# Kernel optimization log

Measured on AMD Instinct MI355X. Metric: run time of the kernel, lower is better.

Reference implementation:

```python
import jax, jax.numpy as jnp
import numpy as np

B, S, H, V, NH, FF, M, NL = 16, 512, 256, 8000, 4, 512, 64, 2
BETA, THR, ALPHA = 0.9, 1.0, 2.0  # snn.Leaky defaults: beta=0.9, threshold=1.0, ATan surrogate alpha=2


@jax.custom_vjp
def spike(u):
    return (u > 0).astype(u.dtype)

def _spike_fwd(u):
    return (u > 0).astype(u.dtype), u

def _spike_bwd(u, g):
    # snntorch ATan surrogate gradient
    return (g * (ALPHA / 2.0) / (1.0 + (jnp.pi * u * ALPHA / 2.0) ** 2),)

spike.defvjp(_spike_fwd, _spike_bwd)


def layer_norm(x, g, b):
    m = x.mean(-1, keepdims=True)
    v = ((x - m) ** 2).mean(-1, keepdims=True)
    return (x - m) / jnp.sqrt(v + 1e-5) * g + b


def mha(x, wqkv, bqkv, wo, bo):
    Bx, Sx, Hx = x.shape
    hd = Hx // NH
    qkv = x @ wqkv.T + bqkv
    q, k, v = jnp.split(qkv, 3, axis=-1)
    sp = lambda t: t.reshape(Bx, Sx, NH, hd).transpose(0, 2, 1, 3)
    q, k, v = sp(q), sp(k), sp(v)
    att = jax.nn.softmax(jnp.einsum('bhqd,bhkd->bhqk', q, k) / (float(hd) ** 0.5), axis=-1)
    o = jnp.einsum('bhqk,bhkd->bhqd', att, v).transpose(0, 2, 1, 3).reshape(Bx, Sx, Hx)
    return o @ wo.T + bo


def spiking_worker(x, w, b):
    # batched projection for all timesteps, then a single-pass LIF scan
    proj = x @ w.T + b  # [B,S,H]

    def step(mem, xt):
        reset = spike(mem - THR)              # spike detected from previous membrane
        mem = BETA * mem + xt - reset * THR   # subtract-reset mechanism
        return mem, spike(mem - THR)

    mem0 = jnp.zeros((x.shape[0], x.shape[2]), x.dtype)
    _, spks = jax.lax.scan(step, mem0, jnp.swapaxes(proj, 0, 1))
    return jnp.swapaxes(spks, 0, 1)  # [B,S,H]


def _forward(input_ids, embed, pos, qkv_w, qkv_b, out_w, out_b, ln1_g, ln1_b,
             ff1_w, ff1_b, ff2_w, ff2_b, ln2_g, ln2_b,
             log_w, log_b, mat_w, mat_b, conv_w, conv_b,
             read_w, read_b, memory, head_w, head_b):
    x = embed[input_ids] + pos[:, :input_ids.shape[1], :]
    for i in range(NL):  # post-norm TransformerEncoderLayer x2, gelu, eval mode
        x = layer_norm(x + mha(x, qkv_w[i], qkv_b[i], out_w[i], out_b[i]), ln1_g[i], ln1_b[i])
        h = jax.nn.gelu(x @ ff1_w[i].T + ff1_b[i], approximate=False) @ ff2_w[i].T + ff2_b[i]
        x = layer_norm(x + h, ln2_g[i], ln2_b[i])
    plan = x
    logico = spiking_worker(plan, log_w, log_b)
    matem = spiking_worker(plan, mat_w, mat_b)
    ling = jax.lax.conv_general_dilated(
        jnp.swapaxes(plan, 1, 2), conv_w, (1,), [(1, 1)],
        dimension_numbers=('NCH', 'OIH', 'NCH')) + conv_b[None, :, None]
    ling = jnp.swapaxes(ling, 1, 2)
    combined = jnp.concatenate([logico, matem, ling, plan], axis=-1)  # [B,S,4H]
    plan_mean = plan.mean(axis=1)                                      # [B,H]
    read_weights = jax.nn.softmax(plan_mean @ read_w.T + read_b, axis=-1)
    memory_read = read_weights @ memory                                # [B,H]
    logits = combined @ head_w.T + head_b                              # [B,S,V]
    return logits, memory_read


def setup_inputs() -> dict:
    key = jax.random.key(0)
    ks = iter(jax.random.split(key, 32))
    sc = 0.02
    rn = lambda shape, s=sc: jax.random.normal(next(ks), shape, jnp.float32) * s
    inp = {
        'input_ids': jax.random.randint(next(ks), (B, S), 0, V),
        'embed': rn((V, H), 1.0),
        'pos': rn((1, 512, H), 1.0),
        'qkv_w': rn((NL, 3 * H, H)), 'qkv_b': rn((NL, 3 * H)),
        'out_w': rn((NL, H, H)), 'out_b': rn((NL, H)),
        'ln1_g': jnp.ones((NL, H), jnp.float32), 'ln1_b': jnp.zeros((NL, H), jnp.float32),
        'ff1_w': rn((NL, FF, H)), 'ff1_b': rn((NL, FF)),
        'ff2_w': rn((NL, H, FF)), 'ff2_b': rn((NL, H)),
        'ln2_g': jnp.ones((NL, H), jnp.float32), 'ln2_b': jnp.zeros((NL, H), jnp.float32),
        'log_w': rn((H, H)), 'log_b': rn((H,)),
        'mat_w': rn((H, H)), 'mat_b': rn((H,)),
        'conv_w': rn((H, H, 3)), 'conv_b': rn((H,)),
        'read_w': rn((M, H)), 'read_b': rn((M,)),
        'memory': rn((M, H), 1.0),
        'head_w': rn((V, 4 * H)), 'head_b': rn((V,)),
    }
    return inp


def reference(input_ids, embed, pos, qkv_w, qkv_b, out_w, out_b, ln1_g, ln1_b,
              ff1_w, ff1_b, ff2_w, ff2_b, ln2_g, ln2_b,
              log_w, log_b, mat_w, mat_b, conv_w, conv_b,
              read_w, read_b, memory, head_w, head_b):
    return _forward(input_ids, embed, pos, qkv_w, qkv_b, out_w, out_b, ln1_g, ln1_b,
                    ff1_w, ff1_b, ff2_w, ff2_b, ln2_g, ln2_b,
                    log_w, log_b, mat_w, mat_b, conv_w, conv_b,
                    read_w, read_b, memory, head_w, head_b)
```

## Files before the change

### kernel.cpp

```cpp
#include <hip/hip_runtime.h>
#include <hip/hip_bf16.h>

constexpr int Bc = 16, Sc = 512, Hc = 256, Vc = 8000, NHc = 4, HDc = 64;
constexpr int FFc = 512, Mc = 64;
constexpr int ROWS = Bc * Sc;
constexpr int CH = 4 * Hc;
constexpr int NT2 = CH / 32;

typedef __attribute__((ext_vector_type(4))) float f32x4v;
typedef __attribute__((ext_vector_type(8))) short short8v;
typedef __hip_bfloat16 bf16;

__device__ inline void split3(float x, bf16& h, bf16& m, bf16& l) {
    h = __float2bfloat16(x);
    const float r = x - __bfloat162float(h);
    m = __float2bfloat16(r);
    const float r2 = r - __bfloat162float(m);
    l = __float2bfloat16(r2);
}

__device__ __forceinline__ void split_range(const float* __restrict__ in,
                                            bf16* __restrict__ h, bf16* __restrict__ m,
                                            bf16* __restrict__ l, int blk, int t) {
    const size_t i = ((size_t)blk * 256 + t) * 4;
    const float4 v = *(const float4*)&in[i];
    split3(v.x, h[i + 0], m[i + 0], l[i + 0]);
    split3(v.y, h[i + 1], m[i + 1], l[i + 1]);
    split3(v.z, h[i + 2], m[i + 2], l[i + 2]);
    split3(v.w, h[i + 3], m[i + 3], l[i + 3]);
}

__global__ __launch_bounds__(256) void k_prep(
    const float* __restrict__ qkv_w, const float* __restrict__ out_w,
    const float* __restrict__ ff1_w, const float* __restrict__ ff2_w,
    const float* __restrict__ log_w, const float* __restrict__ mat_w,
    const float* __restrict__ conv_w, const float* __restrict__ head_w,
    const float* __restrict__ log_b, const float* __restrict__ mat_b,
    bf16* qkvwh, bf16* qkvwm, bf16* qkvwl,
    bf16* outwh, bf16* outwm, bf16* outwl,
    bf16* ff1wh, bf16* ff1wm, bf16* ff1wl,
    bf16* ff2wh, bf16* ff2wm, bf16* ff2wl,
    bf16* lmwh, bf16* lmwm, bf16* lmwl,
    bf16* w2h, bf16* w2m, bf16* w2l,
    bf16* hwb, float* lmb) {
    const int blk = blockIdx.x;
    const int t = threadIdx.x;
    if (blk < 384) {
        split_range(qkv_w, qkvwh, qkvwm, qkvwl, blk, t);
    } else if (blk < 512) {
        split_range(out_w, outwh, outwm, outwl, blk - 384, t);
    } else if (blk < 768) {
        split_range(ff1_w, ff1wh, ff1wm, ff1wl, blk - 512, t);
    } else if (blk < 1024) {
        split_range(ff2_w, ff2wh, ff2wm, ff2wl, blk - 768, t);
    } else if (blk < 1088) {
        split_range(log_w, lmwh, lmwm, lmwl, blk - 1024, t);
    } else if (blk < 1152) {
        split_range(mat_w, lmwh + 65536, lmwm + 65536, lmwl + 65536, blk - 1088, t);
    } else if (blk < 1920) {
        const int idx = (blk - 1152) * 256 + t;
        const int o = idx / 768, rem = idx % 768;
        const int k = rem >> 8, i = rem & 255;
        split3(conv_w[(size_t)o * 768 + i * 3 + k], w2h[idx], w2m[idx], w2l[idx]);
    } else if (blk < 9920) {
        const size_t i = ((size_t)(blk - 1920) * 256 + t) * 4;
        const float4 v = *(const float4*)&head_w[i];
        hwb[i + 0] = __float2bfloat16(v.x);
        hwb[i + 1] = __float2bfloat16(v.y);
        hwb[i + 2] = __float2bfloat16(v.z);
        hwb[i + 3] = __float2bfloat16(v.w);
    } else {
        lmb[t] = log_b[t];
        lmb[256 + t] = mat_b[t];
    }
}

__global__ __launch_bounds__(256) void k_embed(const int* __restrict__ ids,
                                               const float* __restrict__ emb,
                                               const float* __restrict__ pos,
                                               float* __restrict__ x,
                                               bf16* __restrict__ xh, bf16* __restrict__ xm,
                                               bf16* __restrict__ xl) {
    const int r = blockIdx.x;
    const int h = threadIdx.x;
    const int s = r & (Sc - 1);
    const int id = ids[r];
    const float v = emb[(size_t)id * Hc + h] + pos[(size_t)s * Hc + h];
    const size_t o = (size_t)r * Hc + h;
    x[o] = v;
    split3(v, xh[o], xm[o], xl[o]);
}

template <int EPI, int OUTS, int BN>
__global__ __launch_bounds__(256) void k_bg3(
    const bf16* __restrict__ Ah, const bf16* __restrict__ Am, const bf16* __restrict__ Al,
    const bf16* __restrict__ Bh, const bf16* __restrict__ Bm, const bf16* __restrict__ Bl,
    const float* __restrict__ bias, float* __restrict__ C,
    bf16* __restrict__ Oh, bf16* __restrict__ Om, bf16* __restrict__ Ol,
    int K, int lda, int ldb, int ldc,
    long zA2, long zA1, long zB2, long zB1, long zC2, long zC1) {
    constexpr int NF = BN / 32;
    __shared__ bf16 As[3][128 * 32];
    __shared__ bf16 Bs[3][BN * 32];
    const int z = blockIdx.z, z2 = z >> 2, z1 = z & 3;
    const size_t aoff = (size_t)z2 * zA2 + (size_t)z1 * zA1;
    const size_t boff = (size_t)z2 * zB2 + (size_t)z1 * zB1;
    const size_t coff = (size_t)z2 * zC2 + (size_t)z1 * zC1;
    const int t = threadIdx.x;
    const int tm = blockIdx.x * 128, tn = blockIdx.y * BN;
    const int w = t >> 6, l = t & 63;
    const int wr = w >> 1, wc = w & 1;
    const bf16* Ap[3] = {Ah, Am, Al};
    const bf16* Bp[3] = {Bh, Bm, Bl};
    f32x4v acc[4][NF];
    const f32x4v zero = {0.f, 0.f, 0.f, 0.f};
#pragma unroll
    for (int i = 0; i < 4; ++i)
#pragma unroll
        for (int j = 0; j < NF; ++j) acc[i][j] = zero;

    for (int kt = 0; kt < K; kt += 32) {
#pragma unroll
        for (int p = 0; p < 3; ++p) {
#pragma unroll
            for (int j = 0; j < 2; ++j) {
                const int c = j * 256 + t;
                const int row = c >> 2, kc = c & 3;
                const int skc = kc ^ ((row >> 1) & 3);
                const bf16* ga = Ap[p] + aoff + (size_t)(tm + row) * lda + kt + skc * 8;
                __builtin_amdgcn_global_load_lds((const __attribute__((address_space(1))) void*)ga,
                                                 (__attribute__((address_space(3))) void*)(&As[p][0] + c * 8),
                                                 16, 0, 0);
            }
            if (BN == 128) {
#pragma unroll
                for (int j = 0; j < 2; ++j) {
                    const int c = j * 256 + t;
                    const int row = c >> 2, kc = c & 3;
                    const int skc = kc ^ ((row >> 1) & 3);
                    const bf16* gb = Bp[p] + boff + (size_t)(tn + row) * ldb + kt + skc * 8;
                    __builtin_amdgcn_global_load_lds((const __attribute__((address_space(1))) void*)gb,
                                                     (__attribute__((address_space(3))) void*)(&Bs[p][0] + c * 8),
                                                     16, 0, 0);
                }
            } else {
                const int c = t;
                const int row = c >> 2, kc = c & 3;
                const int skc = kc ^ ((row >> 1) & 3);
                const bf16* gb = Bp[p] + boff + (size_t)(tn + row) * ldb + kt + skc * 8;
                __builtin_amdgcn_global_load_lds((const __attribute__((address_space(1))) void*)gb,
                                                 (__attribute__((address_space(3))) void*)(&Bs[p][0] + c * 8),
                                                 16, 0, 0);
            }
        }
        __syncthreads();
        const int lr = l & 15, lkc = l >> 4;
        short8v af[3][4], bfr[3][NF];
#pragma unroll
        for (int p = 0; p < 3; ++p)
#pragma unroll
            for (int m = 0; m < 4; ++m) {
                const int row = wr * 64 + m * 16 + lr;
                const int sc = lkc ^ ((row >> 1) & 3);
                af[p][m] = *(const short8v*)(&As[p][0] + row * 32 + sc * 8);
            }
#pragma unroll
        for (int p = 0; p < 3; ++p)
#pragma unroll
            for (int n = 0; n < NF; ++n) {
                const int row = wc * (BN / 2) + n * 16 + lr;
                const int sc = lkc ^ ((row >> 1) & 3);
                bfr[p][n] = *(const short8v*)(&Bs[p][0] + row * 32 + sc * 8);
            }
#pragma unroll
        for (int m = 0; m < 4; ++m)
#pragma unroll
            for (int n = 0; n < NF; ++n)
                acc[m][n] = __builtin_amdgcn_mfma_f32_16x16x32_bf16(af[0][m], bfr[0][n], acc[m][n], 0, 0, 0);
#pragma unroll
        for (int m = 0; m < 4; ++m)
#pragma unroll
            for (int n = 0; n < NF; ++n)
                acc[m][n] = __builtin_amdgcn_mfma_f32_16x16x32_bf16(af[0][m], bfr[1][n], acc[m][n], 0, 0, 0);
#pragma unroll
        for (int m = 0; m < 4; ++m)
#pragma unroll
            for (int n = 0; n < NF; ++n)
                acc[m][n] = __builtin_amdgcn_mfma_f32_16x16x32_bf16(af[1][m], bfr[0][n], acc[m][n], 0, 0, 0);
#pragma unroll
        for (int m = 0; m < 4; ++m)
#pragma unroll
            for (int n = 0; n < NF; ++n)
                acc[m][n] = __builtin_amdgcn_mfma_f32_16x16x32_bf16(af[0][m], bfr[2][n], acc[m][n], 0, 0, 0);
#pragma unroll
        for (int m = 0; m < 4; ++m)
#pragma unroll
            for (int n = 0; n < NF; ++n)
                acc[m][n] = __builtin_amdgcn_mfma_f32_16x16x32_bf16(af[2][m], bfr[0][n], acc[m][n], 0, 0, 0);
#pragma unroll
        for (int m = 0; m < 4; ++m)
#pragma unroll
            for (int n = 0; n < NF; ++n)
                acc[m][n] = __builtin_amdgcn_mfma_f32_16x16x32_bf16(af[1][m], bfr[1][n], acc[m][n], 0, 0, 0);
        __syncthreads();
    }
    const int lr = l & 15, lq = (l >> 4) * 4;
#pragma unroll
    for (int n = 0; n < NF; ++n) {
        const int col = tn + wc * (BN / 2) + n * 16 + lr;
        const float bv = (EPI == 0 || EPI == 1) ? bias[col] : 0.0f;
#pragma unroll
        for (int m = 0; m < 4; ++m) {
            const int rbase = tm + wr * 64 + m * 16 + lq;
#pragma unroll
            for (int j = 0; j < 4; ++j) {
                float v = acc[m][n][j];
                if (EPI == 0) v += bv;
                if (EPI == 1) { v += bv; v = 0.5f * v * (1.0f + erff(v / 1.41421356237309515f)); }
                const size_t o = coff + (size_t)(rbase + j) * ldc + col;
                if (OUTS == 0) C[o] = v;
                else if (OUTS == 3) ((bf16*)C)[o] = __float2bfloat16(v);
                else split3(v, Oh[o], Om[o], Ol[o]);
            }
        }
    }
}

__global__ __launch_bounds__(256) void k_vt(const bf16* __restrict__ qh,
                                            const bf16* __restrict__ qm,
                                            const bf16* __restrict__ ql,
                                            bf16* __restrict__ vh, bf16* __restrict__ vm,
                                            bf16* __restrict__ vl) {
    __shared__ bf16 tile[64][72];
    const int sblk = blockIdx.x;
    const int z = blockIdx.y;
    const int b = z >> 2, h = z & 3;
    const int t = threadIdx.x;
    const int sr = t >> 2, c16 = (t & 3) * 16;
    const bf16* qp[3] = {qh, qm, ql};
    bf16* vp[3] = {vh, vm, vl};
    for (int p = 0; p < 3; ++p) {
        const bf16* src = qp[p] + (size_t)(b * Sc + sblk * 64 + sr) * 768 + 512 + h * 64 + c16;
        *(short8v*)&tile[sr][c16] = *(const short8v*)src;
        *(short8v*)&tile[sr][c16 + 8] = *(const short8v*)(src + 8);
        __syncthreads();
        bf16 out[16];
#pragma unroll
        for (int i = 0; i < 16; ++i) out[i] = tile[c16 + i][sr];
        bf16* dst = vp[p] + (size_t)(z * 64 + sr) * Sc + sblk * 64 + c16;
        *(short8v*)dst = *(short8v*)&out[0];
        *(short8v*)(dst + 8) = *(short8v*)&out[8];
        __syncthreads();
    }
}

#define S_PASS(QA, KB)                                                                     \
    _Pragma("unroll") for (int m = 0; m < 2; ++m) _Pragma("unroll") for (int ks = 0; ks < 2; ++ks) \
        sa[m] = __builtin_amdgcn_mfma_f32_16x16x32_bf16(QA[m][ks], KB[ks], sa[m], 0, 0, 0);
#define PV_PASS(PA, VB)                                                                    \
    _Pragma("unroll") for (int m = 0; m < 2; ++m) _Pragma("unroll") for (int ks = 0; ks < 2; ++ks) \
        oa[m] = __builtin_amdgcn_mfma_f32_16x16x32_bf16(PA[m][ks], VB[ks], oa[m], 0, 0, 0);

__global__ __launch_bounds__(512) void k_attn(
    const bf16* __restrict__ qph, const bf16* __restrict__ qpm, const bf16* __restrict__ qpl,
    const bf16* __restrict__ vth, const bf16* __restrict__ vtm, const bf16* __restrict__ vtl,
    bf16* __restrict__ oh, bf16* __restrict__ om, bf16* __restrict__ ol) {
    extern __shared__ char smem[];
    float* S = (float*)smem;
    bf16* KV0 = (bf16*)(smem + 131072);
    bf16* KV1 = KV0 + 4096;
    bf16* KV2 = KV1 + 4096;
    const int qc = blockIdx.x, z = blockIdx.y;
    const int b = z >> 2, hh = z & 3;
    const int t = threadIdx.x;
    const int w = t >> 6, lane = t & 63;
    const int lr = lane & 15, lkc = lane >> 4;
    const int qg = w >> 2, kg = w & 3;
    const int r8 = t >> 3, c8 = t & 7;
    const f32x4v zero = {0.f, 0.f, 0.f, 0.f};

    short8v qf0[2][2], qf1[2][2], qf2[2][2];
#pragma unroll
    for (int m = 0; m < 2; ++m)
#pragma unroll
        for (int ks = 0; ks < 2; ++ks) {
            const size_t rbase = (size_t)(b * 512 + qc * 64 + qg * 32 + m * 16 + lr) * 768 + hh * 64 + ks * 32 + lkc * 8;
            qf0[m][ks] = *(const short8v*)(qph + rbase);
            qf1[m][ks] = *(const short8v*)(qpm + rbase);
            qf2[m][ks] = *(const short8v*)(qpl + rbase);
        }

    {
        const size_t srow = (size_t)(b * 512 + 0 * 64 + r8) * 768 + 256 + hh * 64 + (c8 ^ (r8 & 7)) * 8;
        __builtin_amdgcn_global_load_lds((const __attribute__((address_space(1))) void*)(qph + srow),
                                         (__attribute__((address_space(3))) void*)(KV0 + r8 * 64 + c8 * 8), 16, 0, 0);
        __builtin_amdgcn_global_load_lds((const __attribute__((address_space(1))) void*)(qpm + srow),
                                         (__attribute__((address_space(3))) void*)(KV1 + r8 * 64 + c8 * 8), 16, 0, 0);
        __builtin_amdgcn_global_load_lds((const __attribute__((address_space(1))) void*)(qpl + srow),
                                         (__attribute__((address_space(3))) void*)(KV2 + r8 * 64 + c8 * 8), 16, 0, 0);
    }

    for (int kv = 0; kv < 8; ++kv) {
        __syncthreads();
        short8v kb0[2], kb1[2], kb2[2];
#pragma unroll
        for (int ks = 0; ks < 2; ++ks) {
            const int row = kg * 16 + lr;
            const int sc = (ks * 4 + lkc) ^ (row & 7);
            kb0[ks] = *(const short8v*)(KV0 + row * 64 + sc * 8);
            kb1[ks] = *(const short8v*)(KV1 + row * 64 + sc * 8);
            kb2[ks] = *(const short8v*)(KV2 + row * 64 + sc * 8);
        }
        __syncthreads();
        if (kv < 7) {
            const size_t srow = (size_t)(b * 512 + (kv + 1) * 64 + r8) * 768 + 256 + hh * 64 + (c8 ^ (r8 & 7)) * 8;
            __builtin_amdgcn_global_load_lds((const __attribute__((address_space(1))) void*)(qph + srow),
                                             (__attribute__((address_space(3))) void*)(KV0 + r8 * 64 + c8 * 8), 16, 0, 0);
            __builtin_amdgcn_global_load_lds((const __attribute__((address_space(1))) void*)(qpm + srow),
                                             (__attribute__((address_space(3))) void*)(KV1 + r8 * 64 + c8 * 8), 16, 0, 0);
            __builtin_amdgcn_global_load_lds((const __attribute__((address_space(1))) void*)(qpl + srow),
                                             (__attribute__((address_space(3))) void*)(KV2 + r8 * 64 + c8 * 8), 16, 0, 0);
        } else {
            const size_t srow = (size_t)(z * 64 + r8) * 512 + 0 * 64 + (c8 ^ (r8 & 7)) * 8;
            __builtin_amdgcn_global_load_lds((const __attribute__((address_space(1))) void*)(vth + srow),
                                             (__attribute__((address_space(3))) void*)(KV0 + r8 * 64 + c8 * 8), 16, 0, 0);
            __builtin_amdgcn_global_load_lds((const __attribute__((address_space(1))) void*)(vtm + srow),
                                             (__attribute__((address_space(3))) void*)(KV1 + r8 * 64 + c8 * 8), 16, 0, 0);
            __builtin_amdgcn_global_load_lds((const __attribute__((address_space(1))) void*)(vtl + srow),
                                             (__attribute__((address_space(3))) void*)(KV2 + r8 * 64 + c8 * 8), 16, 0, 0);
        }
        f32x4v sa[2] = {zero, zero};
        S_PASS(qf0, kb0) S_PASS(qf0, kb1) S_PASS(qf1, kb0)
        S_PASS(qf0, kb2) S_PASS(qf2, kb0) S_PASS(qf1, kb1)
#pragma unroll
        for (int m = 0; m < 2; ++m)
#pragma unroll
            for (int j = 0; j < 4; ++j) {
                const int row = qg * 32 + m * 16 + (lane >> 4) * 4 + j;
                const int col = kv * 64 + kg * 16 + lr;
                const int chunk = (col >> 2) ^ (row & 7);
                *(float*)((char*)S + row * 2048 + chunk * 16 + (col & 3) * 4) = sa[m][j] * 0.125f;
            }
    }
    __syncthreads();

    for (int r = 0; r < 8; ++r) {
        const int row = w * 8 + r;
        char* rowp = (char*)S + row * 2048;
        const int sw = row & 7;
        float4 x0 = *(float4*)(rowp + ((2 * lane) ^ sw) * 16);
        float4 x1 = *(float4*)(rowp + ((2 * lane + 1) ^ sw) * 16);
        float mx = fmaxf(fmaxf(fmaxf(x0.x, x0.y), fmaxf(x0.z, x0.w)),
                         fmaxf(fmaxf(x1.x, x1.y), fmaxf(x1.z, x1.w)));
#pragma unroll
        for (int d = 1; d < 64; d <<= 1) mx = fmaxf(mx, __shfl_xor(mx, d));
        const float e0 = expf(x0.x - mx), e1 = expf(x0.y - mx), e2 = expf(x0.z - mx), e3 = expf(x0.w - mx);
        const float e4 = expf(x1.x - mx), e5 = expf(x1.y - mx), e6 = expf(x1.z - mx), e7 = expf(x1.w - mx);
        float sm = ((e0 + e1) + (e2 + e3)) + ((e4 + e5) + (e6 + e7));
#pragma unroll
        for (int d = 1; d < 64; d <<= 1) sm += __shfl_xor(sm, d);
        x0.x = e0 / sm; x0.y = e1 / sm; x0.z = e2 / sm; x0.w = e3 / sm;
        x1.x = e4 / sm; x1.y = e5 / sm; x1.z = e6 / sm; x1.w = e7 / sm;
        *(float4*)(rowp + ((2 * lane) ^ sw) * 16) = x0;
        *(float4*)(rowp + ((2 * lane + 1) ^ sw) * 16) = x1;
    }
    __syncthreads();

    f32x4v oa[2] = {zero, zero};
    for (int kv = 0; kv < 8; ++kv) {
        if (kv > 0) __syncthreads();
        short8v vb0[2], vb1[2], vb2[2];
#pragma unroll
        for (int ks = 0; ks < 2; ++ks) {
            const int rowd = kg * 16 + lr;
            const int sc = (ks * 4 + lkc) ^ (rowd & 7);
            vb0[ks] = *(const short8v*)(KV0 + rowd * 64 + sc * 8);
            vb1[ks] = *(const short8v*)(KV1 + rowd * 64 + sc * 8);
            vb2[ks] = *(const short8v*)(KV2 + rowd * 64 + sc * 8);
        }
        __syncthreads();
        if (kv < 7) {
            const size_t srow = (size_t)(z * 64 + r8) * 512 + (kv + 1) * 64 + (c8 ^ (r8 & 7)) * 8;
            __builtin_amdgcn_global_load_lds((const __attribute__((address_space(1))) void*)(vth + srow),
                                             (__attribute__((address_space(3))) void*)(KV0 + r8 * 64 + c8 * 8), 16, 0, 0);
            __builtin_amdgcn_global_load_lds((const __attribute__((address_space(1))) void*)(vtm + srow),
                                             (__attribute__((address_space(3))) void*)(KV1 + r8 * 64 + c8 * 8), 16, 0, 0);
            __builtin_amdgcn_global_load_lds((const __attribute__((address_space(1))) void*)(vtl + srow),
                                             (__attribute__((address_space(3))) void*)(KV2 + r8 * 64 + c8 * 8), 16, 0, 0);
        }
        short8v pah[2][2], pam[2][2], pal[2][2];
#pragma unroll
        for (int m = 0; m < 2; ++m)
#pragma unroll
            for (int ks = 0; ks < 2; ++ks) {
                const int row = qg * 32 + m * 16 + lr;
                const int c0 = kv * 16 + ks * 8 + lkc * 2;
                char* rp = (char*)S + row * 2048;
                const float4 y0 = *(const float4*)(rp + (c0 ^ (row & 7)) * 16);
                const float4 y1 = *(const float4*)(rp + ((c0 + 1) ^ (row & 7)) * 16);
                const float yy[8] = {y0.x, y0.y, y0.z, y0.w, y1.x, y1.y, y1.z, y1.w};
                short8v hv, mv, lv;
#pragma unroll
                for (int i = 0; i < 8; ++i) {
                    bf16 a, bq, c;
                    split3(yy[i], a, bq, c);
                    hv[i] = *(const short*)&a; mv[i] = *(const short*)&bq; lv[i] = *(const short*)&c;
                }
                pah[m][ks] = hv; pam[m][ks] = mv; pal[m][ks] = lv;
            }
        PV_PASS(pah, vb0) PV_PASS(pah, vb1) PV_PASS(pam, vb0)
        PV_PASS(pah, vb2) PV_PASS(pal, vb0) PV_PASS(pam, vb1)
    }
#pragma unroll
    for (int m = 0; m < 2; ++m)
#pragma unroll
        for (int j = 0; j < 4; ++j) {
            const int grow = b * 512 + qc * 64 + qg * 32 + m * 16 + (lane >> 4) * 4 + j;
            const int col = hh * 64 + kg * 16 + lr;
            const size_t o = (size_t)grow * 256 + col;
            split3(oa[m][j], oh[o], om[o], ol[o]);
        }
}

__global__ __launch_bounds__(256) void k_add_ln(float* __restrict__ x,
                                                const float* __restrict__ res,
                                                const float* __restrict__ g,
                                                const float* __restrict__ b,
                                                bf16* __restrict__ xh, bf16* __restrict__ xm,
                                                bf16* __restrict__ xl,
                                                bf16* __restrict__ comb) {
    const size_t row = blockIdx.x;
    const int t = threadIdx.x;
    float v = x[row * Hc + t] + res[row * Hc + t];
    __shared__ float red[256];
    red[t] = v;
    __syncthreads();
    for (int s = 128; s > 0; s >>= 1) { if (t < s) red[t] += red[t + s]; __syncthreads(); }
    const float mean = red[0] * (1.0f / 256.0f);
    __syncthreads();
    const float d = v - mean;
    red[t] = d * d;
    __syncthreads();
    for (int s = 128; s > 0; s >>= 1) { if (t < s) red[t] += red[t + s]; __syncthreads(); }
    const float var = red[0] * (1.0f / 256.0f);
    const float out = d / sqrtf(var + 1e-5f) * g[t] + b[t];
    const size_t o = row * Hc + t;
    x[o] = out;
    split3(out, xh[o], xm[o], xl[o]);
    if (comb != nullptr) comb[row * CH + 768 + t] = __float2bfloat16(out);
}

__global__ __launch_bounds__(256) void k_lif2(const float* __restrict__ lm,
                                              bf16* __restrict__ comb) {
    const int b = blockIdx.x;
    const int half = blockIdx.y;
    const int h = threadIdx.x;
    const float* p = lm + (size_t)b * Sc * 512 + half * 256 + h;
    bf16* o = comb + (size_t)b * Sc * CH + half * 256 + h;
    float mem = 0.0f;
    for (int s0 = 0; s0 < Sc; s0 += 4) {
        float xs[4];
#pragma unroll
        for (int q = 0; q < 4; ++q) xs[q] = p[(size_t)(s0 + q) * 512];
#pragma unroll
        for (int q = 0; q < 4; ++q) {
            const float reset = (mem > 1.0f) ? 1.0f : 0.0f;
            float t1 = 0.9f * mem;
            asm volatile("" : "+v"(t1));
            float t2 = t1 + xs[q];
            asm volatile("" : "+v"(t2));
            mem = t2 - reset;
            o[(size_t)(s0 + q) * CH] = __float2bfloat16((mem > 1.0f) ? 1.0f : 0.0f);
        }
    }
}

__global__ __launch_bounds__(256) void k_aext3(const bf16* __restrict__ xh,
                                               const bf16* __restrict__ xm,
                                               const bf16* __restrict__ xl,
                                               bf16* __restrict__ aeh, bf16* __restrict__ aem,
                                               bf16* __restrict__ ael) {
    const int row = blockIdx.x;
    const int t = threadIdx.x;
    const int b = row >> 9, s = row & 511;
    const bf16 z = __float2bfloat16(0.0f);
#pragma unroll
    for (int k = 0; k < 3; ++k) {
        const int ss = s + k - 1;
        const size_t dst = (size_t)row * 768 + k * 256 + t;
        if (ss >= 0 && ss < Sc) {
            const size_t src = (size_t)(b * Sc + ss) * Hc + t;
            aeh[dst] = xh[src]; aem[dst] = xm[src]; ael[dst] = xl[src];
        } else {
            aeh[dst] = z; aem[dst] = z; ael[dst] = z;
        }
    }
}

__device__ __forceinline__ void stageA32(const bf16* __restrict__ g, int rbase,
                                         bf16* lbase, int kt, int t) {
#pragma unroll
    for (int q = 0; q < 2; ++q) {
        const int f = q * 256 + t;
        const int rowt = f >> 2, chunk = f & 3;
        const int sch = chunk ^ ((rowt >> 1) & 3);
        const bf16* gp = g + (size_t)(rbase + rowt) * CH + kt * 32 + sch * 8;
        __builtin_amdgcn_global_load_lds((const __attribute__((address_space(1))) void*)gp,
                                         (__attribute__((address_space(3))) void*)(lbase + rowt * 32 + chunk * 8),
                                         16, 0, 0);
    }
}
__device__ __forceinline__ void stageB32(const bf16* __restrict__ g, int rbase, int rmax,
                                         bf16* lbase, int kt, int t) {
#pragma unroll
    for (int q = 0; q < 4; ++q) {
        const int f = q * 256 + t;
        const int rowt = f >> 2, chunk = f & 3;
        const int sch = chunk ^ ((rowt >> 1) & 3);
        int grow = rbase + rowt;
        if (grow > rmax) grow = rmax;
        const bf16* gp = g + (size_t)grow * CH + kt * 32 + sch * 8;
        __builtin_amdgcn_global_load_lds((const __attribute__((address_space(1))) void*)gp,
                                         (__attribute__((address_space(3))) void*)(lbase + rowt * 32 + chunk * 8),
                                         16, 0, 0);
    }
}

__global__ __launch_bounds__(256, 2) void k_head8(const bf16* __restrict__ Abf,
                                                  const bf16* __restrict__ Bbf,
                                                  const float* __restrict__ bias,
                                                  float* __restrict__ C) {
    __shared__ bf16 LA[2][128 * 32];
    __shared__ bf16 LB[2][256 * 32];
    const int t = threadIdx.x;
    const int w = t >> 6, lane = t & 63;
    const int wn = w;
    const int tm = blockIdx.x * 128, tn = blockIdx.y * 256;
    const int lr = lane & 15, lkc = lane >> 4;

    f32x4v acc[8][4];
    const f32x4v zero = {0.f, 0.f, 0.f, 0.f};
#pragma unroll
    for (int m = 0; m < 8; ++m)
#pragma unroll
        for (int n = 0; n < 4; ++n) acc[m][n] = zero;

    stageA32(Abf, tm, LA[0], 0, t);
    stageB32(Bbf, tn, Vc - 1, LB[0], 0, t);
    stageA32(Abf, tm, LA[1], 1, t);
    asm volatile("s_waitcnt vmcnt(2)" ::: "memory");
    __builtin_amdgcn_s_barrier();
    __builtin_amdgcn_sched_barrier(0);

    for (int kt = 0; kt < NT2; ++kt) {
        bf16* la = LA[kt & 1];
        bf16* lb = LB[kt & 1];
        bf16* lbN = LB[(kt + 1) & 1];
        short8v a[8], b[4];
#pragma unroll
        for (int m = 0; m < 8; ++m) {
            const int row = m * 16 + lr;
            const int sc = lkc ^ ((row >> 1) & 3);
            a[m] = *(const short8v*)(la + row * 32 + sc * 8);
        }
#pragma unroll
        for (int n = 0; n < 4; ++n) {
            const int row = wn * 64 + n * 16 + lr;
            const int sc = lkc ^ ((row >> 1) & 3);
            b[n] = *(const short8v*)(lb + row * 32 + sc * 8);
        }
        if (kt + 1 < NT2) stageB32(Bbf, tn, Vc - 1, lbN, kt + 1, t);
        __builtin_amdgcn_s_barrier();
        __builtin_amdgcn_sched_barrier(0);
        __builtin_amdgcn_s_setprio(1);
#pragma unroll
        for (int m = 0; m < 8; ++m)
#pragma unroll
            for (int n = 0; n < 2; ++n)
                acc[m][n] = __builtin_amdgcn_mfma_f32_16x16x32_bf16(a[m], b[n], acc[m][n], 0, 0, 0);
        __builtin_amdgcn_s_setprio(0);
        __builtin_amdgcn_s_barrier();
        __builtin_amdgcn_sched_barrier(0);
        if (kt + 2 < NT2) stageA32(Abf, tm, la, kt + 2, t);
        __builtin_amdgcn_s_setprio(1);
#pragma unroll
        for (int m = 0; m < 8; ++m)
#pragma unroll
            for (int n = 2; n < 4; ++n)
                acc[m][n] = __builtin_amdgcn_mfma_f32_16x16x32_bf16(a[m], b[n], acc[m][n], 0, 0, 0);
        __builtin_amdgcn_s_setprio(0);
        if (kt + 2 < NT2) asm volatile("s_waitcnt vmcnt(2)" ::: "memory");
        else              asm volatile("s_waitcnt vmcnt(0)" ::: "memory");
        __builtin_amdgcn_s_barrier();
        __builtin_amdgcn_sched_barrier(0);
    }
    const int lq = (lane >> 4) * 4;
#pragma unroll
    for (int n = 0; n < 4; ++n) {
        const int col = tn + wn * 64 + n * 16 + lr;
        if (col >= Vc) continue;
        const float bv = bias[col];
#pragma unroll
        for (int m = 0; m < 8; ++m) {
            const int rbase = tm + m * 16 + lq;
#pragma unroll
            for (int j = 0; j < 4; ++j)
                C[(size_t)(rbase + j) * Vc + col] = acc[m][n][j] + bv;
        }
    }
}

__global__ __launch_bounds__(256) void k_pmean(const float* __restrict__ plan, float* __restrict__ pm2) {
    const int b = blockIdx.x, c = blockIdx.y;
    const int h = threadIdx.x;
    const float* p = plan + ((size_t)(b * Sc + c * 64)) * Hc + h;
    float s = 0.0f;
    for (int i = 0; i < 64; ++i) s += p[(size_t)i * Hc];
    pm2[((size_t)b * 8 + c) * Hc + h] = s;
}

__global__ __launch_bounds__(256) void k_memread(const float* __restrict__ pm2,
                                                 const float* __restrict__ rw,
                                                 const float* __restrict__ rb,
                                                 const float* __restrict__ memm,
                                                 float* __restrict__ out) {
    const int b = blockIdx.x;
    const int t = threadIdx.x;
    __shared__ float pms[256];
    __shared__ float lg[64];
    __shared__ float sm[64];
    float v = 0.0f;
    for (int c = 0; c < 8; ++c) v += pm2[((size_t)b * 8 + c) * Hc + t];
    pms[t] = v * (1.0f / 512.0f);
    __syncthreads();
    if (t < 64) {
        float s = rb[t];
        const float* wrow = rw + (size_t)t * Hc;
        for (int i = 0; i < Hc; ++i) s = fmaf(wrow[i], pms[i], s);
        lg[t] = s;
    }
    __syncthreads();
    if (t == 0) {
        float mx = lg[0];
        for (int i = 1; i < 64; ++i) mx = fmaxf(mx, lg[i]);
        float ssum = 0.0f;
        for (int i = 0; i < 64; ++i) { const float e = expf(lg[i] - mx); sm[i] = e; ssum += e; }
        for (int i = 0; i < 64; ++i) sm[i] /= ssum;
    }
    __syncthreads();
    float s = 0.0f;
    for (int m = 0; m < 64; ++m) s = fmaf(sm[m], memm[(size_t)m * Hc + t], s);
    out[(size_t)b * Hc + t] = s;
}

extern "C" void kernel_launch(void* const* d_in, const int* in_sizes, int n_in,
                              void* d_out, int out_size, void* d_ws, size_t ws_size,
                              hipStream_t stream) {
    const int*   ids    = (const int*)  d_in[0];
    const float* embed  = (const float*)d_in[1];
    const float* pos    = (const float*)d_in[2];
    const float* qkv_w  = (const float*)d_in[3];
    const float* qkv_b  = (const float*)d_in[4];
    const float* out_w  = (const float*)d_in[5];
    const float* out_b  = (const float*)d_in[6];
    const float* ln1_g  = (const float*)d_in[7];
    const float* ln1_b  = (const float*)d_in[8];
    const float* ff1_w  = (const float*)d_in[9];
    const float* ff1_b  = (const float*)d_in[10];
    const float* ff2_w  = (const float*)d_in[11];
    const float* ff2_b  = (const float*)d_in[12];
    const float* ln2_g  = (const float*)d_in[13];
    const float* ln2_b  = (const float*)d_in[14];
    const float* log_w  = (const float*)d_in[15];
    const float* log_b  = (const float*)d_in[16];
    const float* mat_w  = (const float*)d_in[17];
    const float* mat_b  = (const float*)d_in[18];
    const float* conv_w = (const float*)d_in[19];
    const float* conv_b = (const float*)d_in[20];
    const float* read_w = (const float*)d_in[21];
    const float* read_b = (const float*)d_in[22];
    const float* memory = (const float*)d_in[23];
    const float* head_w = (const float*)d_in[24];
    const float* head_b = (const float*)d_in[25];

    char* wsb = (char*)d_ws;
    const size_t MB = 1ull << 20;
    float* X    = (float*)(wsb + 0);
    bf16*  XH   = (bf16*)(wsb + 8 * MB);
    bf16*  XM   = (bf16*)(wsb + 12 * MB);
    bf16*  XL   = (bf16*)(wsb + 16 * MB);
    float* RES  = (float*)(wsb + 20 * MB);
    bf16*  QPH  = (bf16*)(wsb + 28 * MB);
    bf16*  QPM  = (bf16*)(wsb + 40 * MB);
    bf16*  QPL  = (bf16*)(wsb + 52 * MB);
    bf16*  OH   = (bf16*)(wsb + 64 * MB);
    bf16*  OM   = (bf16*)(wsb + 68 * MB);
    bf16*  OL   = (bf16*)(wsb + 72 * MB);
    bf16*  VTH  = (bf16*)(wsb + 76 * MB);
    bf16*  VTM  = (bf16*)(wsb + 80 * MB);
    bf16*  VTL  = (bf16*)(wsb + 84 * MB);
    bf16*  H1H  = (bf16*)(wsb + 88 * MB);
    bf16*  H1M  = (bf16*)(wsb + 96 * MB);
    bf16*  H1L  = (bf16*)(wsb + 104 * MB);
    float* LOGMAT = (float*)(wsb + 76 * MB);
    bf16*  AEH  = (bf16*)(wsb + 92 * MB);
    bf16*  AEM  = (bf16*)(wsb + 104 * MB);
    bf16*  AEL  = (bf16*)(wsb + 116 * MB);
    bf16*  COMB = (bf16*)(wsb + 128 * MB);
    bf16*  HWB  = (bf16*)(wsb + 144 * MB);
    bf16*  WP   = (bf16*)(wsb + 160 * MB);
    float* PM2  = (float*)(wsb + 64 * MB);

    float* logits = (float*)d_out;
    float* mread  = logits + (size_t)ROWS * Vc;

    bf16* qkvwh = WP;             bf16* qkvwm = qkvwh + 393216; bf16* qkvwl = qkvwm + 393216;
    bf16* outwh = qkvwl + 393216; bf16* outwm = outwh + 131072; bf16* outwl = outwm + 131072;
    bf16* ff1wh = outwl + 131072; bf16* ff1wm = ff1wh + 262144; bf16* ff1wl = ff1wm + 262144;
    bf16* ff2wh = ff1wl + 262144; bf16* ff2wm = ff2wh + 262144; bf16* ff2wl = ff2wm + 262144;
    bf16* lmwh  = ff2wl + 262144; bf16* lmwm  = lmwh + 131072;  bf16* lmwl  = lmwm + 131072;
    bf16* w2h   = lmwl + 131072;  bf16* w2m   = w2h + 196608;   bf16* w2l   = w2m + 196608;
    float* LMB  = (float*)(w2l + 196608);

    hipFuncSetAttribute((const void*)k_attn, hipFuncAttributeMaxDynamicSharedMemorySize, 155648);

    k_prep<<<dim3(9921), 256, 0, stream>>>(
        qkv_w, out_w, ff1_w, ff2_w, log_w, mat_w, conv_w, head_w, log_b, mat_b,
        qkvwh, qkvwm, qkvwl, outwh, outwm, outwl, ff1wh, ff1wm, ff1wl,
        ff2wh, ff2wm, ff2wl, lmwh, lmwm, lmwl, w2h, w2m, w2l, HWB, LMB);

    k_embed<<<dim3(ROWS), 256, 0, stream>>>(ids, embed, pos, X, XH, XM, XL);
    for (int l = 0; l < 2; ++l) {
        k_bg3<0, 1, 128><<<dim3(64, 6, 1), 256, 0, stream>>>(
            XH, XM, XL,
            qkvwh + (size_t)l * 196608, qkvwm + (size_t)l * 196608, qkvwl + (size_t)l * 196608,
            qkv_b + l * 768, nullptr, QPH, QPM, QPL,
            256, 256, 256, 768, 0, 0, 0, 0, 0, 0);
        k_vt<<<dim3(8, 64), 256, 0, stream>>>(QPH, QPM, QPL, VTH, VTM, VTL);
        k_attn<<<dim3(8, 64), 512, 155648, stream>>>(QPH, QPM, QPL, VTH, VTM, VTL, OH, OM, OL);
        k_bg3<0, 0, 64><<<dim3(64, 4, 1), 256, 0, stream>>>(
            OH, OM, OL,
            outwh + (size_t)l * 65536, outwm + (size_t)l * 65536, outwl + (size_t)l * 65536,
            out_b + l * 256, RES, nullptr, nullptr, nullptr,
            256, 256, 256, 256, 0, 0, 0, 0, 0, 0);
        k_add_ln<<<dim3(ROWS), 256, 0, stream>>>(X, RES, ln1_g + l * 256, ln1_b + l * 256,
                                                 XH, XM, XL, nullptr);
        k_bg3<1, 1, 128><<<dim3(64, 4, 1), 256, 0, stream>>>(
            XH, XM, XL,
            ff1wh + (size_t)l * 131072, ff1wm + (size_t)l * 131072, ff1wl + (size_t)l * 131072,
            ff1_b + l * 512, nullptr, H1H, H1M, H1L,
            256, 256, 256, 512, 0, 0, 0, 0, 0, 0);
        k_bg3<0, 0, 64><<<dim3(64, 4, 1), 256, 0, stream>>>(
            H1H, H1M, H1L,
            ff2wh + (size_t)l * 131072, ff2wm + (size_t)l * 131072, ff2wl + (size_t)l * 131072,
            ff2_b + l * 256, RES, nullptr, nullptr, nullptr,
            512, 512, 512, 256, 0, 0, 0, 0, 0, 0);
        k_add_ln<<<dim3(ROWS), 256, 0, stream>>>(X, RES, ln2_g + l * 256, ln2_b + l * 256,
                                                 XH, XM, XL, (l == 1) ? COMB : nullptr);
    }
    k_bg3<0, 0, 128><<<dim3(64, 4, 1), 256, 0, stream>>>(
        XH, XM, XL, lmwh, lmwm, lmwl, LMB, LOGMAT, nullptr, nullptr, nullptr,
        256, 256, 256, 512, 0, 0, 0, 0, 0, 0);
    k_aext3<<<dim3(ROWS), 256, 0, stream>>>(XH, XM, XL, AEH, AEM, AEL);
    k_lif2<<<dim3(Bc, 2), 256, 0, stream>>>(LOGMAT, COMB);
    k_bg3<0, 3, 64><<<dim3(64, 4, 1), 256, 0, stream>>>(
        AEH, AEM, AEL, w2h, w2m, w2l, conv_b, (float*)(COMB + 512), nullptr, nullptr, nullptr,
        768, 768, 768, CH, 0, 0, 0, 0, 0, 0);
    k_head8<<<dim3(64, 32), 256, 0, stream>>>(COMB, HWB, head_b, logits);
    k_pmean<<<dim3(Bc, 8), 256, 0, stream>>>(X, PM2);
    k_memread<<<dim3(Bc), 256, 0, stream>>>(PM2, read_w, read_b, memory, mread);
}
```

Baseline: 756.6 us.

## Vectorize bf16 stores, widen LIF unroll, raise head occupancy bound

The head-weight bf16 conversion now writes four values with one 8-byte store. The conv im2col kernel is rewritten so each thread moves four elements with vector loads and stores, and its launch grid is resized to 6144 blocks to match. The serial LIF scan prefetches eight timesteps per iteration instead of four, giving more memory-level parallelism on the single-thread-per-channel recurrence. The head GEMM launch bound moves from 2 to 3 waves per SIMD, which may force register spilling for the 8x4 accumulator tile.

```diff
diff --git a/kernel.cpp b/kernel.cpp
--- a/kernel.cpp
+++ b/kernel.cpp
@@ -9,6 +9,7 @@
 
 typedef __attribute__((ext_vector_type(4))) float f32x4v;
 typedef __attribute__((ext_vector_type(8))) short short8v;
+typedef __attribute__((ext_vector_type(4))) short short4v;
 typedef __hip_bfloat16 bf16;
 
 __device__ inline void split3(float x, bf16& h, bf16& m, bf16& l) {
@@ -65,10 +66,12 @@
     } else if (blk < 9920) {
         const size_t i = ((size_t)(blk - 1920) * 256 + t) * 4;
         const float4 v = *(const float4*)&head_w[i];
-        hwb[i + 0] = __float2bfloat16(v.x);
-        hwb[i + 1] = __float2bfloat16(v.y);
-        hwb[i + 2] = __float2bfloat16(v.z);
-        hwb[i + 3] = __float2bfloat16(v.w);
+        bf16 b0 = __float2bfloat16(v.x), b1 = __float2bfloat16(v.y);
+        bf16 b2 = __float2bfloat16(v.z), b3 = __float2bfloat16(v.w);
+        short4v sv;
+        sv[0] = *(const short*)&b0; sv[1] = *(const short*)&b1;
+        sv[2] = *(const short*)&b2; sv[3] = *(const short*)&b3;
+        *(short4v*)(hwb + i) = sv;
     } else {
         lmb[t] = log_b[t];
         lmb[256 + t] = mat_b[t];
@@ -458,12 +461,12 @@
     const float* p = lm + (size_t)b * Sc * 512 + half * 256 + h;
     bf16* o = comb + (size_t)b * Sc * CH + half * 256 + h;
     float mem = 0.0f;
-    for (int s0 = 0; s0 < Sc; s0 += 4) {
-        float xs[4];
-#pragma unroll
-        for (int q = 0; q < 4; ++q) xs[q] = p[(size_t)(s0 + q) * 512];
-#pragma unroll
-        for (int q = 0; q < 4; ++q) {
+    for (int s0 = 0; s0 < Sc; s0 += 8) {
+        float xs[8];
+#pragma unroll
+        for (int q = 0; q < 8; ++q) xs[q] = p[(size_t)(s0 + q) * 512];
+#pragma unroll
+        for (int q = 0; q < 8; ++q) {
             const float reset = (mem > 1.0f) ? 1.0f : 0.0f;
             float t1 = 0.9f * mem;
             asm volatile("" : "+v"(t1));
@@ -480,20 +483,23 @@
                                                const bf16* __restrict__ xl,
                                                bf16* __restrict__ aeh, bf16* __restrict__ aem,
                                                bf16* __restrict__ ael) {
-    const int row = blockIdx.x;
-    const int t = threadIdx.x;
+    const int idx = blockIdx.x * 256 + threadIdx.x;
+    const int row = idx / 192, c4 = idx % 192;
+    const int c = c4 * 4;
+    const int k = c >> 8, i = c & 255;
     const int b = row >> 9, s = row & 511;
-    const bf16 z = __float2bfloat16(0.0f);
-#pragma unroll
-    for (int k = 0; k < 3; ++k) {
-        const int ss = s + k - 1;
-        const size_t dst = (size_t)row * 768 + k * 256 + t;
-        if (ss >= 0 && ss < Sc) {
-            const size_t src = (size_t)(b * Sc + ss) * Hc + t;
-            aeh[dst] = xh[src]; aem[dst] = xm[src]; ael[dst] = xl[src];
-        } else {
-            aeh[dst] = z; aem[dst] = z; ael[dst] = z;
-        }
+    const int ss = s + k - 1;
+    const size_t dst = (size_t)row * 768 + c;
+    if (ss >= 0 && ss < Sc) {
+        const size_t src = (size_t)(b * Sc + ss) * Hc + i;
+        *(short4v*)(aeh + dst) = *(const short4v*)(xh + src);
+        *(short4v*)(aem + dst) = *(const short4v*)(xm + src);
+        *(short4v*)(ael + dst) = *(const short4v*)(xl + src);
+    } else {
+        const short4v z = {0, 0, 0, 0};
+        *(short4v*)(aeh + dst) = z;
+        *(short4v*)(aem + dst) = z;
+        *(short4v*)(ael + dst) = z;
     }
 }
 
@@ -526,7 +532,7 @@
     }
 }
 
-__global__ __launch_bounds__(256, 2) void k_head8(const bf16* __restrict__ Abf,
+__global__ __launch_bounds__(256, 3) void k_head8(const bf16* __restrict__ Abf,
                                                   const bf16* __restrict__ Bbf,
                                                   const float* __restrict__ bias,
                                                   float* __restrict__ C) {
@@ -761,7 +767,7 @@
     k_bg3<0, 0, 128><<<dim3(64, 4, 1), 256, 0, stream>>>(
         XH, XM, XL, lmwh, lmwm, lmwl, LMB, LOGMAT, nullptr, nullptr, nullptr,
         256, 256, 256, 512, 0, 0, 0, 0, 0, 0);
-    k_aext3<<<dim3(ROWS), 256, 0, stream>>>(XH, XM, XL, AEH, AEM, AEL);
+    k_aext3<<<dim3(6144), 256, 0, stream>>>(XH, XM, XL, AEH, AEM, AEL);
     k_lif2<<<dim3(Bc, 2), 256, 0, stream>>>(LOGMAT, COMB);
     k_bg3<0, 3, 64><<<dim3(64, 4, 1), 256, 0, stream>>>(
         AEH, AEM, AEL, w2h, w2m, w2l, conv_b, (float*)(COMB + 512), nullptr, nullptr, nullptr,
```

Result: slower. 1.226 ms (median of 2 runs) (+62.0%).
